# Kernel tuning notes

Hardware: AMD Instinct MI355X
Metric: run time of the kernel (lower is better)

## Reference

```python
import jax, jax.numpy as jnp
import numpy as np

B, H, L, D = 2, 8, 512, 64
TEMP = 8.0  # sqrt(D)


def setup_inputs() -> dict:
    key = jax.random.key(0)
    ks = jax.random.split(key, 6)
    q = jax.random.normal(ks[0], (B, H, L, D), jnp.float32)
    k = jax.random.normal(ks[1], (B, H, L, D), jnp.float32)
    v = jax.random.normal(ks[2], (B, H, L, D), jnp.float32)
    adj_k = jax.random.normal(ks[3], (B, L, L, D), jnp.float32)
    adj_v = jax.random.normal(ks[4], (B, L, L, D), jnp.float32)
    mask = jax.random.randint(ks[5], (B, 1, 1, L), 0, 2, jnp.int32)
    return {"q": q, "k": k, "v": v, "adj_k": adj_k, "adj_v": adj_v, "mask": mask}


def reference(q, k, v, adj_k, adj_v, mask):
    qs = q / TEMP
    # standard QK^T term + relation term: score[b,h,i,j] += q[b,h,i]. adj_k[b,i,j]
    attn = jnp.einsum('bhid,bhjd->bhij', qs, k) + jnp.einsum('bhid,bijd->bhij', qs, adj_k)
    attn = jnp.where(mask == 0, jnp.float32(-10000.0), attn)
    attn = jax.nn.softmax(attn, axis=-1)  # dropout p=0 (eval / deterministic)
    # standard AV term + relation term: out[b,h,i] += sum_j attn[b,h,i,j]*adj_v[b,i,j]
    out = jnp.einsum('bhij,bhjd->bhid', attn, v) + jnp.einsum('bhij,bijd->bhid', attn, adj_v)
    return out, attn
```

## Files before the change

kernel.cpp:

```cpp
#include <hip/hip_runtime.h>

constexpr int B  = 2;
constexpr int NH = 8;
constexpr int L  = 512;
constexpr int D  = 64;
constexpr float INV_TEMP = 0.125f;

__global__ __launch_bounds__(256) void k1_qk(const float* __restrict__ q,
                                             const float* __restrict__ k,
                                             float* __restrict__ s1) {
  const int bh = blockIdx.x, it = blockIdx.y, jt = blockIdx.z;
  __shared__ float Qs[64][68];
  __shared__ float Ks[128][68];
  const int t = threadIdx.x;
  const float* qb = q + ((size_t)bh * L + it * 64) * D;
  const float* kb = k + ((size_t)bh * L + jt * 128) * D;
#pragma unroll
  for (int n0 = 0; n0 < 4; ++n0) {
    int n = t + (n0 << 8);
    int r = n >> 4, c = (n & 15) << 2;
    float4 a = *(const float4*)(qb + (size_t)r * D + c);
    a.x *= INV_TEMP; a.y *= INV_TEMP; a.z *= INV_TEMP; a.w *= INV_TEMP;
    *(float4*)&Qs[r][c] = a;
  }
#pragma unroll
  for (int n0 = 0; n0 < 8; ++n0) {
    int n = t + (n0 << 8);
    int r = n >> 4, c = (n & 15) << 2;
    *(float4*)&Ks[r][c] = *(const float4*)(kb + (size_t)r * D + c);
  }
  __syncthreads();
  const int i0 = t >> 4, j0 = t & 15;
  float acc[4][8] = {};
#pragma unroll 1
  for (int kc = 0; kc < 64; kc += 4) {
    float4 a[4], b[8];
#pragma unroll
    for (int m = 0; m < 4; ++m) a[m] = *(const float4*)&Qs[i0 + 16 * m][kc];
#pragma unroll
    for (int n = 0; n < 8; ++n) b[n] = *(const float4*)&Ks[j0 + 16 * n][kc];
#pragma unroll
    for (int m = 0; m < 4; ++m)
#pragma unroll
      for (int n = 0; n < 8; ++n)
        acc[m][n] = fmaf(a[m].x, b[n].x,
                    fmaf(a[m].y, b[n].y,
                    fmaf(a[m].z, b[n].z,
                    fmaf(a[m].w, b[n].w, acc[m][n]))));
  }
  float* sb = s1 + ((size_t)bh * L + it * 64) * L + jt * 128;
#pragma unroll
  for (int m = 0; m < 4; ++m) {
    float* srow = sb + (size_t)(i0 + 16 * m) * L;
#pragma unroll
    for (int n = 0; n < 8; ++n) srow[j0 + 16 * n] = acc[m][n];
  }
}

__global__ __launch_bounds__(256) void k2_fused(
    const float* __restrict__ q, const float* __restrict__ k,
    const float* __restrict__ v, const float* __restrict__ adj_k,
    const float* __restrict__ adj_v, const int* __restrict__ mask,
    const float* __restrict__ s1, float* __restrict__ out,
    float* __restrict__ attn) {
  const int b = blockIdx.x >> 9, i = blockIdx.x & (L - 1);
  const int t = threadIdx.x;
  const int lane = t & 63;
  const int hp = __builtin_amdgcn_readfirstlane(t >> 6);
  __shared__ float sc[NH][L];
  __shared__ float ak[64][65];

  const float* akb  = adj_k + ((size_t)b * L + i) * (size_t)L * D;
  const float* qr0  = q + (((size_t)b * NH + hp    ) * L + i) * D;
  const float* qr1  = q + (((size_t)b * NH + hp + 4) * L + i) * D;
  const float* s1r0 = s1 + (((size_t)b * NH + hp    ) * L + i) * L;
  const float* s1r1 = s1 + (((size_t)b * NH + hp + 4) * L + i) * L;

  for (int jc = 0; jc < L; jc += 64) {
    __syncthreads();
#pragma unroll
    for (int n0 = 0; n0 < 4; ++n0) {
      int n = t + (n0 << 8);
      int r = n >> 4, c = (n & 15) << 2;
      float4 a = *(const float4*)(akb + (size_t)(jc + r) * D + c);
      ak[r][c] = a.x; ak[r][c + 1] = a.y; ak[r][c + 2] = a.z; ak[r][c + 3] = a.w;
    }
    __syncthreads();
    float acc0 = 0.f, acc1 = 0.f;
#pragma unroll
    for (int dc = 0; dc < D; dc += 4) {
      float a0 = ak[lane][dc],     a1 = ak[lane][dc + 1];
      float a2 = ak[lane][dc + 2], a3 = ak[lane][dc + 3];
      float4 q0 = *(const float4*)(qr0 + dc);
      float4 q1 = *(const float4*)(qr1 + dc);
      acc0 = fmaf(q0.x, a0, fmaf(q0.y, a1, fmaf(q0.z, a2, fmaf(q0.w, a3, acc0))));
      acc1 = fmaf(q1.x, a0, fmaf(q1.y, a1, fmaf(q1.z, a2, fmaf(q1.w, a3, acc1))));
    }
    sc[hp    ][jc + lane] = s1r0[jc + lane] + acc0 * INV_TEMP;
    sc[hp + 4][jc + lane] = s1r1[jc + lane] + acc1 * INV_TEMP;
  }
  __syncthreads();

  {
    const int h = t >> 5, l = t & 31;
    const int* mrow = mask + b * L;
    float* arow = attn + (((size_t)b * NH + h) * L + i) * L;
    float vals[16];
    float mx = -3.4e38f;
#pragma unroll
    for (int m = 0; m < 16; ++m) {
      int jj = l + (m << 5);
      float vsc = sc[h][jj];
      vsc = (mrow[jj] == 0) ? -10000.0f : vsc;
      vals[m] = vsc;
      mx = fmaxf(mx, vsc);
    }
#pragma unroll
    for (int off = 16; off > 0; off >>= 1) mx = fmaxf(mx, __shfl_xor(mx, off, 32));
    float sum = 0.f;
#pragma unroll
    for (int m = 0; m < 16; ++m) { vals[m] = __expf(vals[m] - mx); sum += vals[m]; }
#pragma unroll
    for (int off = 16; off > 0; off >>= 1) sum += __shfl_xor(sum, off, 32);
    const float inv = 1.0f / sum;
#pragma unroll
    for (int m = 0; m < 16; ++m) {
      int jj = l + (m << 5);
      float p = vals[m] * inv;
      arow[jj] = p;
      sc[h][jj] = p;
    }
  }
  __syncthreads();

  {
    const float* avp = adj_v + ((size_t)b * L + i) * (size_t)L * D + lane;
    const float* v0p = v + ((size_t)b * NH + hp    ) * (size_t)L * D + lane;
    const float* v1p = v + ((size_t)b * NH + hp + 4) * (size_t)L * D + lane;
    float o0 = 0.f, o1 = 0.f;
    for (int jc = 0; jc < L; jc += 64) {
      float p0 = sc[hp    ][jc + lane];
      float p1 = sc[hp + 4][jc + lane];
      const float* ap = avp + (size_t)jc * D;
      const float* w0 = v0p + (size_t)jc * D;
      const float* w1 = v1p + (size_t)jc * D;
#pragma unroll 16
      for (int j = 0; j < 64; ++j) {
        float pj0 = __uint_as_float(__builtin_amdgcn_readlane(__float_as_uint(p0), j));
        float pj1 = __uint_as_float(__builtin_amdgcn_readlane(__float_as_uint(p1), j));
        float av = ap[(size_t)j * D];
        float w0v = w0[(size_t)j * D];
        float w1v = w1[(size_t)j * D];
        o0 = fmaf(pj0, av + w0v, o0);
        o1 = fmaf(pj1, av + w1v, o1);
      }
    }
    const size_t ob = (((size_t)b * NH + hp) * L + i) * D + lane;
    out[ob] = o0;
    out[ob + (size_t)4 * L * D] = o1;
  }
}

extern "C" void kernel_launch(void* const* d_in, const int* in_sizes, int n_in,
                              void* d_out, int out_size, void* d_ws, size_t ws_size,
                              hipStream_t stream) {
  const float* q     = (const float*)d_in[0];
  const float* k     = (const float*)d_in[1];
  const float* v     = (const float*)d_in[2];
  const float* adj_k = (const float*)d_in[3];
  const float* adj_v = (const float*)d_in[4];
  const int*   mask  = (const int*)d_in[5];
  float* out  = (float*)d_out;
  float* attn = out + (size_t)B * NH * L * D;
  float* s1   = (float*)d_ws;

  dim3 g1(B * NH, L / 64, L / 128);
  k1_qk<<<g1, 256, 0, stream>>>(q, k, s1);
  k2_fused<<<B * L, 256, 0, stream>>>(q, k, v, adj_k, adj_v, mask, s1, out, attn);
}
```

Before: 352.9 us.

## Repartition fused kernel work: per-wave key ranges, register-held q, vectorized adj loads

Restructures the fused relation-attention kernel. Each wave now owns a 128-key slice, and lanes are split 8 heads by 8 subgroups. Scaled q lives in registers, and adj_k rows are read directly with float4 loads instead of being staged through shared memory. The AV phase uses float4 loads over 8-wide d slices, and the per-wave partial outputs are reduced through shared memory. This aims to cut shared-memory staging, barriers and scalar loads, at the cost of higher register pressure (q in 64 registers) and a cross-wave reduction step.

```diff
diff --git a/kernel.cpp b/kernel.cpp
--- a/kernel.cpp
+++ b/kernel.cpp
@@ -5,6 +5,7 @@
 constexpr int L  = 512;
 constexpr int D  = 64;
 constexpr float INV_TEMP = 0.125f;
+constexpr int SCP = 520;
 
 __global__ __launch_bounds__(256) void k1_qk(const float* __restrict__ q,
                                              const float* __restrict__ k,
@@ -57,60 +58,59 @@
   }
 }
 
-__global__ __launch_bounds__(256) void k2_fused(
-    const float* __restrict__ q, const float* __restrict__ k,
-    const float* __restrict__ v, const float* __restrict__ adj_k,
-    const float* __restrict__ adj_v, const int* __restrict__ mask,
-    const float* __restrict__ s1, float* __restrict__ out,
-    float* __restrict__ attn) {
+__global__ __launch_bounds__(256, 4) void k2_fused(
+    const float* __restrict__ q, const float* __restrict__ v,
+    const float* __restrict__ adj_k, const float* __restrict__ adj_v,
+    const int* __restrict__ mask, const float* __restrict__ s1,
+    float* __restrict__ out, float* __restrict__ attn) {
   const int b = blockIdx.x >> 9, i = blockIdx.x & (L - 1);
   const int t = threadIdx.x;
-  const int lane = t & 63;
-  const int hp = __builtin_amdgcn_readfirstlane(t >> 6);
-  __shared__ float sc[NH][L];
-  __shared__ float ak[64][65];
+  const int wv = t >> 6, lane = t & 63;
+  const int h = lane >> 3, sub = lane & 7;
+  __shared__ float sc[NH * SCP];
+  __shared__ float obuf[4 * NH * D];
 
-  const float* akb  = adj_k + ((size_t)b * L + i) * (size_t)L * D;
-  const float* qr0  = q + (((size_t)b * NH + hp    ) * L + i) * D;
-  const float* qr1  = q + (((size_t)b * NH + hp + 4) * L + i) * D;
-  const float* s1r0 = s1 + (((size_t)b * NH + hp    ) * L + i) * L;
-  const float* s1r1 = s1 + (((size_t)b * NH + hp + 4) * L + i) * L;
+  const float* qrow = q + (((size_t)b * NH + h) * L + i) * D;
+  float4 qreg[16];
+#pragma unroll
+  for (int u = 0; u < 16; ++u) {
+    float4 qv = *(const float4*)(qrow + 4 * u);
+    qreg[u].x = qv.x * INV_TEMP; qreg[u].y = qv.y * INV_TEMP;
+    qreg[u].z = qv.z * INV_TEMP; qreg[u].w = qv.w * INV_TEMP;
+  }
 
-  for (int jc = 0; jc < L; jc += 64) {
-    __syncthreads();
-#pragma unroll
-    for (int n0 = 0; n0 < 4; ++n0) {
-      int n = t + (n0 << 8);
-      int r = n >> 4, c = (n & 15) << 2;
-      float4 a = *(const float4*)(akb + (size_t)(jc + r) * D + c);
-      ak[r][c] = a.x; ak[r][c + 1] = a.y; ak[r][c + 2] = a.z; ak[r][c + 3] = a.w;
+  const float* akb = adj_k + ((size_t)b * L + i) * (size_t)L * D;
+  const float* s1r = s1 + (((size_t)b * NH + h) * L + i) * L;
+  const int jw = wv * 128;
+  for (int c = 0; c < 16; c += 2) {
+    const int ja = jw + c * 8 + sub, jb = ja + 8;
+    const float* ra = akb + (size_t)ja * D;
+    const float* rb = akb + (size_t)jb * D;
+    float accA = s1r[ja], accB = s1r[jb];
+#pragma unroll 4
+    for (int u = 0; u < 16; ++u) {
+      float4 a = *(const float4*)(ra + 4 * u);
+      float4 bq = *(const float4*)(rb + 4 * u);
+      accA = fmaf(qreg[u].x, a.x, fmaf(qreg[u].y, a.y,
+             fmaf(qreg[u].z, a.z, fmaf(qreg[u].w, a.w, accA))));
+      accB = fmaf(qreg[u].x, bq.x, fmaf(qreg[u].y, bq.y,
+             fmaf(qreg[u].z, bq.z, fmaf(qreg[u].w, bq.w, accB))));
     }
-    __syncthreads();
-    float acc0 = 0.f, acc1 = 0.f;
-#pragma unroll
-    for (int dc = 0; dc < D; dc += 4) {
-      float a0 = ak[lane][dc],     a1 = ak[lane][dc + 1];
-      float a2 = ak[lane][dc + 2], a3 = ak[lane][dc + 3];
-      float4 q0 = *(const float4*)(qr0 + dc);
-      float4 q1 = *(const float4*)(qr1 + dc);
-      acc0 = fmaf(q0.x, a0, fmaf(q0.y, a1, fmaf(q0.z, a2, fmaf(q0.w, a3, acc0))));
-      acc1 = fmaf(q1.x, a0, fmaf(q1.y, a1, fmaf(q1.z, a2, fmaf(q1.w, a3, acc1))));
-    }
-    sc[hp    ][jc + lane] = s1r0[jc + lane] + acc0 * INV_TEMP;
-    sc[hp + 4][jc + lane] = s1r1[jc + lane] + acc1 * INV_TEMP;
+    sc[h * SCP + ja] = accA;
+    sc[h * SCP + jb] = accB;
   }
   __syncthreads();
 
   {
-    const int h = t >> 5, l = t & 31;
+    const int hB = t >> 5, lB = t & 31;
     const int* mrow = mask + b * L;
-    float* arow = attn + (((size_t)b * NH + h) * L + i) * L;
+    float* arow = attn + (((size_t)b * NH + hB) * L + i) * L;
     float vals[16];
     float mx = -3.4e38f;
 #pragma unroll
     for (int m = 0; m < 16; ++m) {
-      int jj = l + (m << 5);
-      float vsc = sc[h][jj];
+      int jj = lB + (m << 5);
+      float vsc = sc[hB * SCP + jj];
       vsc = (mrow[jj] == 0) ? -10000.0f : vsc;
       vals[m] = vsc;
       mx = fmaxf(mx, vsc);
@@ -125,39 +125,56 @@
     const float inv = 1.0f / sum;
 #pragma unroll
     for (int m = 0; m < 16; ++m) {
-      int jj = l + (m << 5);
+      int jj = lB + (m << 5);
       float p = vals[m] * inv;
       arow[jj] = p;
-      sc[h][jj] = p;
+      sc[hB * SCP + jj] = p;
     }
   }
   __syncthreads();
 
   {
-    const float* avp = adj_v + ((size_t)b * L + i) * (size_t)L * D + lane;
-    const float* v0p = v + ((size_t)b * NH + hp    ) * (size_t)L * D + lane;
-    const float* v1p = v + ((size_t)b * NH + hp + 4) * (size_t)L * D + lane;
-    float o0 = 0.f, o1 = 0.f;
-    for (int jc = 0; jc < L; jc += 64) {
-      float p0 = sc[hp    ][jc + lane];
-      float p1 = sc[hp + 4][jc + lane];
-      const float* ap = avp + (size_t)jc * D;
-      const float* w0 = v0p + (size_t)jc * D;
-      const float* w1 = v1p + (size_t)jc * D;
-#pragma unroll 16
-      for (int j = 0; j < 64; ++j) {
-        float pj0 = __uint_as_float(__builtin_amdgcn_readlane(__float_as_uint(p0), j));
-        float pj1 = __uint_as_float(__builtin_amdgcn_readlane(__float_as_uint(p1), j));
-        float av = ap[(size_t)j * D];
-        float w0v = w0[(size_t)j * D];
-        float w1v = w1[(size_t)j * D];
-        o0 = fmaf(pj0, av + w0v, o0);
-        o1 = fmaf(pj1, av + w1v, o1);
-      }
+    const int d0 = sub * 8;
+    const float* avb = adj_v + ((size_t)b * L + i) * (size_t)L * D + d0;
+    const float* vb  = v + ((size_t)b * NH + h) * (size_t)L * D + d0;
+    float4 acA = {0.f, 0.f, 0.f, 0.f}, acB = {0.f, 0.f, 0.f, 0.f};
+    for (int j = jw; j < jw + 128; j += 2) {
+      float p0 = sc[h * SCP + j];
+      float p1 = sc[h * SCP + j + 1];
+      const float* a0 = avb + (size_t)j * D;
+      const float* w0 = vb + (size_t)j * D;
+      float4 av00 = *(const float4*)(a0);
+      float4 av01 = *(const float4*)(a0 + 4);
+      float4 vv00 = *(const float4*)(w0);
+      float4 vv01 = *(const float4*)(w0 + 4);
+      float4 av10 = *(const float4*)(a0 + D);
+      float4 av11 = *(const float4*)(a0 + D + 4);
+      float4 vv10 = *(const float4*)(w0 + D);
+      float4 vv11 = *(const float4*)(w0 + D + 4);
+      acA.x = fmaf(p0, av00.x + vv00.x, acA.x);
+      acA.y = fmaf(p0, av00.y + vv00.y, acA.y);
+      acA.z = fmaf(p0, av00.z + vv00.z, acA.z);
+      acA.w = fmaf(p0, av00.w + vv00.w, acA.w);
+      acB.x = fmaf(p0, av01.x + vv01.x, acB.x);
+      acB.y = fmaf(p0, av01.y + vv01.y, acB.y);
+      acB.z = fmaf(p0, av01.z + vv01.z, acB.z);
+      acB.w = fmaf(p0, av01.w + vv01.w, acB.w);
+      acA.x = fmaf(p1, av10.x + vv10.x, acA.x);
+      acA.y = fmaf(p1, av10.y + vv10.y, acA.y);
+      acA.z = fmaf(p1, av10.z + vv10.z, acA.z);
+      acA.w = fmaf(p1, av10.w + vv10.w, acA.w);
+      acB.x = fmaf(p1, av11.x + vv11.x, acB.x);
+      acB.y = fmaf(p1, av11.y + vv11.y, acB.y);
+      acB.z = fmaf(p1, av11.z + vv11.z, acB.z);
+      acB.w = fmaf(p1, av11.w + vv11.w, acB.w);
     }
-    const size_t ob = (((size_t)b * NH + hp) * L + i) * D + lane;
-    out[ob] = o0;
-    out[ob + (size_t)4 * L * D] = o1;
+    *(float4*)&obuf[(wv * NH * D) + h * D + d0]     = acA;
+    *(float4*)&obuf[(wv * NH * D) + h * D + d0 + 4] = acB;
+  }
+  __syncthreads();
+  for (int n = t; n < NH * D; n += 256) {
+    float s = obuf[n] + obuf[NH * D + n] + obuf[2 * NH * D + n] + obuf[3 * NH * D + n];
+    out[(((size_t)b * NH + (n >> 6)) * L + i) * D + (n & 63)] = s;
   }
 }
 
@@ -176,5 +193,5 @@
 
   dim3 g1(B * NH, L / 64, L / 128);
   k1_qk<<<g1, 256, 0, stream>>>(q, k, s1);
-  k2_fused<<<B * L, 256, 0, stream>>>(q, k, v, adj_k, adj_v, mask, s1, out, attn);
+  k2_fused<<<B * L, 256, 0, stream>>>(q, v, adj_k, adj_v, mask, s1, out, attn);
 }
```

New measurement: 519.0 us. +47.1%, slower.
